# Performance work log

Measured on AMD Instinct MI355X. Metric: run time of the kernel, lower is better.

## Reference

```python
import jax, jax.numpy as jnp
import numpy as np

L, D, H, HD, M = 4096, 1024, 16, 64, 4096
EPS = 1e-5


def setup_inputs() -> dict:
    key = jax.random.key(0)
    ks = jax.random.split(key, 12)
    hidden_states = jax.random.normal(ks[0], (L, D), dtype=jnp.float32)
    cu_seqlens = jnp.arange(5, dtype=jnp.int32) * (L // 4)  # [0,1024,2048,3072,4096]
    # rope freqs as cos/sin of random angles: (L, HD//2, 2)
    angles = jax.random.uniform(ks[1], (L, HD // 2), dtype=jnp.float32) * (2.0 * np.pi)
    rope_freqs = jnp.stack([jnp.cos(angles), jnp.sin(angles)], axis=-1)
    s = 0.02
    params = {
        "ln0_g": jnp.ones((D,), jnp.float32), "ln0_b": jnp.zeros((D,), jnp.float32),
        "ln1_g": jnp.ones((D,), jnp.float32), "ln1_b": jnp.zeros((D,), jnp.float32),
        "w_qkv": jax.random.normal(ks[2], (D, 3 * D), jnp.float32) * s,
        "w_o":   jax.random.normal(ks[3], (D, D), jnp.float32) * s,
        "w_fc0": jax.random.normal(ks[4], (D, M), jnp.float32) * s,
        "b_fc0": jnp.zeros((M,), jnp.float32),
        "w_fc1": jax.random.normal(ks[5], (M, D), jnp.float32) * s,
        "b_fc1": jnp.zeros((D,), jnp.float32),
    }
    return {"hidden_states": hidden_states, "cu_seqlens": cu_seqlens, "rope_freqs": rope_freqs, **params}


def _layernorm(x, g, b):
    mu = jnp.mean(x, axis=-1, keepdims=True)
    var = jnp.var(x, axis=-1, keepdims=True)
    return (x - mu) * jax.lax.rsqrt(var + EPS) * g + b


def _apply_rope(x, fc):
    # x: (L, H, HD); fc: (L, HD//2, 2) -> broadcast over heads
    xr = x.reshape(L, H, HD // 2, 2)
    a, b = xr[..., 0], xr[..., 1]
    c, s = fc[:, None, :, 0], fc[:, None, :, 1]
    out = jnp.stack([a * c - b * s, a * s + b * c], axis=-1)
    return out.reshape(L, H, HD)


def reference(hidden_states, cu_seqlens, rope_freqs, ln0_g, ln0_b, ln1_g, ln1_b,
              w_qkv, w_o, w_fc0, b_fc0, w_fc1, b_fc1):
    residual = hidden_states
    x = _layernorm(hidden_states, ln0_g, ln0_b)
    qkv = (x @ w_qkv).reshape(L, 3, H, HD)
    q, k, v = qkv[:, 0], qkv[:, 1], qkv[:, 2]
    q = _apply_rope(q, rope_freqs)
    k = _apply_rope(k, rope_freqs)
    # block-diagonal mask from cu_seqlens
    seg = jnp.searchsorted(cu_seqlens[1:], jnp.arange(L, dtype=cu_seqlens.dtype), side="right")
    mask = seg[:, None] == seg[None, :]  # (L, L)
    scale = 1.0 / np.sqrt(HD)
    scores = jnp.einsum("lhd,mhd->hlm", q, k) * scale
    scores = jnp.where(mask[None], scores, jnp.float32(-1e30))
    probs = jax.nn.softmax(scores, axis=-1)
    attn = jnp.einsum("hlm,mhd->lhd", probs, v).reshape(L, D)
    attn = attn @ w_o
    h = residual + attn
    y = _layernorm(h, ln1_g, ln1_b)
    y = jax.nn.gelu(y @ w_fc0 + b_fc0, approximate=False) @ w_fc1 + b_fc1
    return h + y
```

## Files before the change

kernel.cpp:

```cpp
#include <hip/hip_runtime.h>
#include <cstdint>
#include <cmath>

#define L_ 4096
#define D_ 1024
#define H_ 16
#define HD_ 64
#define M_ 4096

typedef __bf16 bf16_t;
typedef __attribute__((ext_vector_type(8))) __bf16 bf16x8;
typedef __attribute__((ext_vector_type(4))) __bf16 bf16x4;
typedef __attribute__((ext_vector_type(4))) float f32x4;

__device__ __forceinline__ f32x4 mfma16(bf16x8 a, bf16x8 b, f32x4 c) {
    return __builtin_amdgcn_mfma_f32_16x16x32_bf16(a, b, c, 0, 0, 0);
}

__device__ __forceinline__ void gload_lds16(const bf16_t* g, bf16_t* l) {
    __builtin_amdgcn_global_load_lds(
        (const __attribute__((address_space(1))) unsigned int*)(g),
        (__attribute__((address_space(3))) unsigned int*)(l), 16, 0, 0);
}

__device__ __forceinline__ float fast_exp2(float x) {
    float r;
    asm volatile("v_exp_f32 %0, %1" : "=v"(r) : "v"(x));
    return r;
}
__device__ __forceinline__ float fast_rcp(float x) {
    float r;
    asm volatile("v_rcp_f32 %0, %1" : "=v"(r) : "v"(x));
    return r;
}
__device__ __forceinline__ float gelu_f(float v) {
    float t = v * (0.7978845608f + 0.0356774081f * v * v);
    return v * fast_rcp(1.f + fast_exp2(-2.885390082f * t));
}

__global__ __launch_bounds__(256) void ln_kernel(const float* __restrict__ x,
                                                 const float* __restrict__ g,
                                                 const float* __restrict__ b,
                                                 bf16_t* __restrict__ out) {
    int row = blockIdx.x, tid = threadIdx.x;
    int wave = tid >> 6, lane = tid & 63;
    const f32x4* xr = (const f32x4*)(x + (long)row * D_);
    f32x4 v = xr[tid];
    float s = v.x + v.y + v.z + v.w;
    __shared__ float red[8];
#pragma unroll
    for (int off = 32; off > 0; off >>= 1) s += __shfl_down(s, off, 64);
    if (lane == 0) red[wave] = s;
    __syncthreads();
    float mean = (red[0] + red[1] + red[2] + red[3]) * (1.f / 1024.f);
    float s2 = 0.f;
#pragma unroll
    for (int i = 0; i < 4; i++) { float d = v[i] - mean; s2 += d * d; }
#pragma unroll
    for (int off = 32; off > 0; off >>= 1) s2 += __shfl_down(s2, off, 64);
    __syncthreads();
    if (lane == 0) red[wave] = s2;
    __syncthreads();
    float var = (red[0] + red[1] + red[2] + red[3]) * (1.f / 1024.f);
    float rstd = rsqrtf(var + 1e-5f);
    f32x4 g4 = ((const f32x4*)g)[tid];
    f32x4 b4 = ((const f32x4*)b)[tid];
    bf16x4 o;
#pragma unroll
    for (int i = 0; i < 4; i++) o[i] = (bf16_t)((v[i] - mean) * rstd * g4[i] + b4[i]);
    *(bf16x4*)(out + (long)row * D_ + tid * 4) = o;
}

__global__ __launch_bounds__(256) void transpose_all(
    const float* __restrict__ w_qkv, const float* __restrict__ w_o,
    const float* __restrict__ w_fc0, const float* __restrict__ w_fc1,
    bf16_t* __restrict__ t_qkv, bf16_t* __restrict__ t_o,
    bf16_t* __restrict__ t_fc0, bf16_t* __restrict__ t_fc1) {
    __shared__ float t[32][33];
    int bidx = blockIdx.x;
    const float* W;
    bf16_t* Wt;
    int K, N, tile;
    if (bidx < 3072) { W = w_qkv; Wt = t_qkv; K = 1024; N = 3072; tile = bidx; }
    else if (bidx < 4096) { W = w_o; Wt = t_o; K = 1024; N = 1024; tile = bidx - 3072; }
    else if (bidx < 8192) { W = w_fc0; Wt = t_fc0; K = 1024; N = 4096; tile = bidx - 4096; }
    else { W = w_fc1; Wt = t_fc1; K = 4096; N = 1024; tile = bidx - 8192; }
    int nt = N >> 5;
    int n0 = (tile % nt) * 32, k0 = (tile / nt) * 32;
    int tx = threadIdx.x & 31, ty = threadIdx.x >> 5;
#pragma unroll
    for (int r = 0; r < 32; r += 8)
        t[ty + r][tx] = W[(long)(k0 + ty + r) * N + n0 + tx];
    __syncthreads();
#pragma unroll
    for (int r = 0; r < 32; r += 8)
        Wt[(long)(n0 + ty + r) * K + k0 + tx] = (bf16_t)t[tx][ty + r];
}

__global__ __launch_bounds__(256) void vt_kernel(const bf16_t* __restrict__ qkv,
                                                 bf16_t* __restrict__ Vt) {
    __shared__ bf16_t t[32][33];
    int l0 = blockIdx.x * 32, c0 = blockIdx.y * 32;
    int tx = threadIdx.x & 31, ty = threadIdx.x >> 5;
#pragma unroll
    for (int r = 0; r < 32; r += 8)
        t[ty + r][tx] = qkv[(long)(l0 + ty + r) * 3072 + 2048 + c0 + tx];
    __syncthreads();
#pragma unroll
    for (int r = 0; r < 32; r += 8)
        Vt[(long)(c0 + ty + r) * 4096 + l0 + tx] = t[tx][ty + r];
}

__global__ __launch_bounds__(256) void rope_kernel(bf16_t* __restrict__ qkv,
                                                   const float* __restrict__ freqs) {
    const float k1 = 0.125f * 1.44269504089f;
    int idx = blockIdx.x * 256 + threadIdx.x;
    int g = idx & 7;
    int h = (idx >> 3) & 15;
    int l = idx >> 7;
    const float* f = freqs + (long)l * 64 + g * 8;
    f32x4 f0 = ((const f32x4*)f)[0];
    f32x4 f1 = ((const f32x4*)f)[1];
    float c[4] = {f0.x, f0.z, f1.x, f1.z};
    float s[4] = {f0.y, f0.w, f1.y, f1.w};
    bf16_t* qp = qkv + (long)l * 3072 + h * 64 + g * 8;
    bf16x8 q = *(bf16x8*)qp;
    bf16x8 k = *(bf16x8*)(qp + 1024);
    bf16x8 qo, ko;
#pragma unroll
    for (int e = 0; e < 4; e++) {
        float a = (float)q[2 * e], b = (float)q[2 * e + 1];
        qo[2 * e] = (bf16_t)((a * c[e] - b * s[e]) * k1);
        qo[2 * e + 1] = (bf16_t)((a * s[e] + b * c[e]) * k1);
        a = (float)k[2 * e]; b = (float)k[2 * e + 1];
        ko[2 * e] = (bf16_t)(a * c[e] - b * s[e]);
        ko[2 * e + 1] = (bf16_t)(a * s[e] + b * c[e]);
    }
    *(bf16x8*)qp = qo;
    *(bf16x8*)(qp + 1024) = ko;
}

template <int EPI, int GN, int SWBN, int SWBM>
__global__ __launch_bounds__(256) void gemm_bt(const bf16_t* __restrict__ A,
                                               const bf16_t* __restrict__ Bt,
                                               int M, int N, int K,
                                               bf16_t* __restrict__ outB,
                                               const float* __restrict__ bias) {
    __shared__ __align__(16) bf16_t As[128 * 64];
    __shared__ __align__(16) bf16_t Bs[128 * 64];
    int tid = threadIdx.x;
    int wave = tid >> 6, lane = tid & 63;
    int quad = lane >> 4, l16 = lane & 15;
    int wr = wave >> 1, wc = wave & 1;

    int g = blockIdx.x & 7, w = blockIdx.x >> 3;
    int gn_idx = g % GN, gm_idx = g / GN;
    int bn_i = gn_idx * SWBN + (w % SWBN);
    int bm_i = gm_idx * SWBM + (w / SWBN);
    long bm = (long)bm_i * 128, bn = (long)bn_i * 128;

    f32x4 acc[4][4];
#pragma unroll
    for (int i = 0; i < 4; i++)
#pragma unroll
        for (int j = 0; j < 4; j++) acc[i][j] = (f32x4){0.f, 0.f, 0.f, 0.f};

    int lr = lane >> 3;
    int sc = (lane & 7) ^ (lr & 7);
    const bf16_t* a_base = A + (bm + wave * 32 + lr) * (long)K + sc * 8;
    const bf16_t* b_base = Bt + (bn + wave * 32 + lr) * (long)K + sc * 8;

    for (int k0 = 0; k0 < K; k0 += 64) {
        __syncthreads();
#pragma unroll
        for (int i = 0; i < 4; i++) {
            gload_lds16(a_base + k0 + (long)(8 * i) * K, &As[(wave * 32 + 8 * i) * 64]);
            gload_lds16(b_base + k0 + (long)(8 * i) * K, &Bs[(wave * 32 + 8 * i) * 64]);
        }
        __builtin_amdgcn_s_waitcnt(0);
        __syncthreads();

#pragma unroll
        for (int h = 0; h < 2; h++) {
            int sl = (h * 4 + quad) ^ (l16 & 7);
            bf16x8 af[4], bfr[4];
#pragma unroll
            for (int i = 0; i < 4; i++) {
                af[i] = *(const bf16x8*)&As[(wr * 64 + i * 16 + l16) * 64 + sl * 8];
                bfr[i] = *(const bf16x8*)&Bs[(wc * 64 + i * 16 + l16) * 64 + sl * 8];
            }
#pragma unroll
            for (int i = 0; i < 4; i++)
#pragma unroll
                for (int j = 0; j < 4; j++)
                    acc[i][j] = mfma16(af[i], bfr[j], acc[i][j]);
        }
    }

    long base_row = bm + wr * 64;
    long base_col = bn + wc * 64;
#pragma unroll
    for (int i = 0; i < 4; i++)
#pragma unroll
        for (int j = 0; j < 4; j++)
#pragma unroll
            for (int r = 0; r < 4; r++) {
                long row = base_row + i * 16 + quad * 4 + r;
                long col = base_col + j * 16 + l16;
                long idx = row * (long)N + col;
                float v = acc[i][j][r];
                if (EPI == 0) {
                    outB[idx] = (bf16_t)v;
                } else {
                    v += bias[col];
                    outB[idx] = (bf16_t)gelu_f(v);
                }
            }
}

__global__ __launch_bounds__(256) void gemm_splitk_store(const bf16_t* __restrict__ A,
                                                         const bf16_t* __restrict__ Bt,
                                                         int M, int N, int K, int Kc,
                                                         bf16_t* __restrict__ P) {
    __shared__ __align__(16) bf16_t As[128 * 64];
    __shared__ __align__(16) bf16_t Bs[128 * 64];
    int tid = threadIdx.x;
    int wave = tid >> 6, lane = tid & 63;
    int quad = lane >> 4, l16 = lane & 15;
    int wr = wave >> 1, wc = wave & 1;

    int g = blockIdx.x & 7, w = blockIdx.x >> 3;
    int z = g & 3, bm_hi = g >> 2;
    int bn_i = w & 7, bm_i = bm_hi * 16 + (w >> 3);
    long bm = (long)bm_i * 128, bn = (long)bn_i * 128;
    int kbeg = z * Kc, kend = kbeg + Kc;
    bf16_t* myP = P + (long)z * M * N;

    f32x4 acc[4][4];
#pragma unroll
    for (int i = 0; i < 4; i++)
#pragma unroll
        for (int j = 0; j < 4; j++) acc[i][j] = (f32x4){0.f, 0.f, 0.f, 0.f};

    int lr = lane >> 3;
    int sc = (lane & 7) ^ (lr & 7);
    const bf16_t* a_base = A + (bm + wave * 32 + lr) * (long)K + sc * 8;
    const bf16_t* b_base = Bt + (bn + wave * 32 + lr) * (long)K + sc * 8;

    for (int k0 = kbeg; k0 < kend; k0 += 64) {
        __syncthreads();
#pragma unroll
        for (int i = 0; i < 4; i++) {
            gload_lds16(a_base + k0 + (long)(8 * i) * K, &As[(wave * 32 + 8 * i) * 64]);
            gload_lds16(b_base + k0 + (long)(8 * i) * K, &Bs[(wave * 32 + 8 * i) * 64]);
        }
        __builtin_amdgcn_s_waitcnt(0);
        __syncthreads();

#pragma unroll
        for (int h = 0; h < 2; h++) {
            int sl = (h * 4 + quad) ^ (l16 & 7);
            bf16x8 af[4], bfr[4];
#pragma unroll
            for (int i = 0; i < 4; i++) {
                af[i] = *(const bf16x8*)&As[(wr * 64 + i * 16 + l16) * 64 + sl * 8];
                bfr[i] = *(const bf16x8*)&Bs[(wc * 64 + i * 16 + l16) * 64 + sl * 8];
            }
#pragma unroll
            for (int i = 0; i < 4; i++)
#pragma unroll
                for (int j = 0; j < 4; j++)
                    acc[i][j] = mfma16(af[i], bfr[j], acc[i][j]);
        }
    }

    long base_row = bm + wr * 64;
    long base_col = bn + wc * 64;
#pragma unroll
    for (int i = 0; i < 4; i++)
#pragma unroll
        for (int j = 0; j < 4; j++)
#pragma unroll
            for (int r = 0; r < 4; r++) {
                long row = base_row + i * 16 + quad * 4 + r;
                long col = base_col + j * 16 + l16;
                myP[row * (long)N + col] = (bf16_t)acc[i][j][r];
            }
}

__global__ __launch_bounds__(256) void reduce_fc1(const bf16_t* __restrict__ P,
                                                  const float* __restrict__ bias,
                                                  float* __restrict__ out) {
    long i = (long)blockIdx.x * 256 + threadIdx.x;
    f32x4 b = ((const f32x4*)bias)[i & 255];
    f32x4 v = ((f32x4*)out)[i];
#pragma unroll
    for (int z = 0; z < 4; z++) {
        bf16x4 p = ((const bf16x4*)(P + (long)z * L_ * D_))[i];
#pragma unroll
        for (int e = 0; e < 4; e++) v[e] += (float)p[e];
    }
    v.x += b.x; v.y += b.y; v.z += b.z; v.w += b.w;
    ((f32x4*)out)[i] = v;
}

__global__ __launch_bounds__(256) void gemm_bt64_res(const bf16_t* __restrict__ A,
                                                     const bf16_t* __restrict__ Bt,
                                                     int M, int N, int K,
                                                     float* __restrict__ outF,
                                                     const float* __restrict__ res) {
    __shared__ __align__(16) bf16_t As[128 * 64];
    __shared__ __align__(16) bf16_t Bs[64 * 64];
    int tid = threadIdx.x;
    int wave = tid >> 6, lane = tid & 63;
    int quad = lane >> 4, l16 = lane & 15;

    int g = blockIdx.x & 7, w = blockIdx.x >> 3;
    int bn_i = w & 15, bm_i = g * 4 + (w >> 4);
    long bm = (long)bm_i * 128, bn = (long)bn_i * 64;

    f32x4 acc[2][4];
#pragma unroll
    for (int i = 0; i < 2; i++)
#pragma unroll
        for (int j = 0; j < 4; j++) acc[i][j] = (f32x4){0.f, 0.f, 0.f, 0.f};

    int lr = lane >> 3;
    int sc = (lane & 7) ^ (lr & 7);
    const bf16_t* a_base = A + (bm + wave * 32 + lr) * (long)K + sc * 8;
    const bf16_t* b_base = Bt + (bn + wave * 16 + lr) * (long)K + sc * 8;

    for (int k0 = 0; k0 < K; k0 += 64) {
        __syncthreads();
#pragma unroll
        for (int i = 0; i < 4; i++)
            gload_lds16(a_base + k0 + (long)(8 * i) * K, &As[(wave * 32 + 8 * i) * 64]);
#pragma unroll
        for (int i = 0; i < 2; i++)
            gload_lds16(b_base + k0 + (long)(8 * i) * K, &Bs[(wave * 16 + 8 * i) * 64]);
        __builtin_amdgcn_s_waitcnt(0);
        __syncthreads();

#pragma unroll
        for (int h = 0; h < 2; h++) {
            int sl = (h * 4 + quad) ^ (l16 & 7);
            bf16x8 af[2], bfr[4];
#pragma unroll
            for (int i = 0; i < 2; i++)
                af[i] = *(const bf16x8*)&As[(wave * 32 + i * 16 + l16) * 64 + sl * 8];
#pragma unroll
            for (int j = 0; j < 4; j++)
                bfr[j] = *(const bf16x8*)&Bs[(j * 16 + l16) * 64 + sl * 8];
#pragma unroll
            for (int i = 0; i < 2; i++)
#pragma unroll
                for (int j = 0; j < 4; j++)
                    acc[i][j] = mfma16(af[i], bfr[j], acc[i][j]);
        }
    }

#pragma unroll
    for (int i = 0; i < 2; i++)
#pragma unroll
        for (int j = 0; j < 4; j++)
#pragma unroll
            for (int r = 0; r < 4; r++) {
                long row = bm + wave * 32 + i * 16 + quad * 4 + r;
                long col = bn + j * 16 + l16;
                long idx = row * (long)N + col;
                outF[idx] = acc[i][j][r] + res[idx];
            }
}

__global__ __launch_bounds__(256) void attn_kernel(const bf16_t* __restrict__ qkv,
                                                   const bf16_t* __restrict__ Vt,
                                                   const int* __restrict__ cu,
                                                   bf16_t* __restrict__ out) {
    __shared__ __align__(16) bf16_t QPs[4 * 16 * 72];
    __shared__ __align__(16) bf16_t Ks[64 * 64];
    __shared__ __align__(16) bf16_t Vs[64 * 64];

    int tid = threadIdx.x, wave = tid >> 6, lane = tid & 63;
    int quad = lane >> 4, l16 = lane & 15;
    int qt = blockIdx.x, head = blockIdx.y, seg = blockIdx.z;
    int s0 = cu[seg], s1 = cu[seg + 1];
    int r0 = s0 + qt * 64;
    const long hoff = (long)head * 64;

    bf16_t* Qs = QPs;
    bf16_t* Psw = &QPs[wave * 16 * 72];

    int lr = lane >> 3;
    int sc = (lane & 7) ^ (lr & 7);
    int sl0 = (0 * 4 + quad) ^ (l16 & 7);
    int sl1 = (1 * 4 + quad) ^ (l16 & 7);

#pragma unroll
    for (int i = 0; i < 2; i++) {
        int row = wave * 16 + i * 8 + lr;
        gload_lds16(qkv + (long)(r0 + row) * 3072 + hoff + sc * 8,
                    &Qs[(wave * 16 + i * 8) * 64]);
    }
    __builtin_amdgcn_s_waitcnt(0);
    __syncthreads();
    bf16x8 aq0 = *(const bf16x8*)&Qs[(wave * 16 + l16) * 64 + sl0 * 8];
    bf16x8 aq1 = *(const bf16x8*)&Qs[(wave * 16 + l16) * 64 + sl1 * 8];

    bf16x8 ones;
#pragma unroll
    for (int e = 0; e < 8; e++) ones[e] = (bf16_t)1.0f;

    f32x4 o[4];
#pragma unroll
    for (int j = 0; j < 4; j++) o[j] = (f32x4){0.f, 0.f, 0.f, 0.f};
    f32x4 lacc = (f32x4){0.f, 0.f, 0.f, 0.f};

    for (int kt = s0; kt < s1; kt += 64) {
        __syncthreads();
#pragma unroll
        for (int i = 0; i < 2; i++) {
            int row = wave * 16 + i * 8 + lr;
            gload_lds16(qkv + (long)(kt + row) * 3072 + 1024 + hoff + sc * 8,
                        &Ks[(wave * 16 + i * 8) * 64]);
            gload_lds16(Vt + (hoff + row) * (long)4096 + kt + sc * 8,
                        &Vs[(wave * 16 + i * 8) * 64]);
        }
        __builtin_amdgcn_s_waitcnt(0);
        __syncthreads();

        f32x4 sacc[4];
#pragma unroll
        for (int j = 0; j < 4; j++) sacc[j] = (f32x4){0.f, 0.f, 0.f, 0.f};
#pragma unroll
        for (int j = 0; j < 4; j++) {
            bf16x8 b0 = *(const bf16x8*)&Ks[(j * 16 + l16) * 64 + sl0 * 8];
            bf16x8 b1 = *(const bf16x8*)&Ks[(j * 16 + l16) * 64 + sl1 * 8];
            sacc[j] = mfma16(aq0, b0, sacc[j]);
            sacc[j] = mfma16(aq1, b1, sacc[j]);
        }

#pragma unroll
        for (int j = 0; j < 4; j++)
#pragma unroll
            for (int r = 0; r < 4; r++)
                Psw[(quad * 4 + r) * 72 + j * 16 + l16] = (bf16_t)fast_exp2(sacc[j][r]);

        __builtin_amdgcn_s_waitcnt(0);

        bf16x8 ap0 = *(const bf16x8*)&Psw[l16 * 72 + 0 * 32 + quad * 8];
        bf16x8 ap1 = *(const bf16x8*)&Psw[l16 * 72 + 1 * 32 + quad * 8];
#pragma unroll
        for (int j2 = 0; j2 < 4; j2++) {
            bf16x8 b0 = *(const bf16x8*)&Vs[(j2 * 16 + l16) * 64 + sl0 * 8];
            bf16x8 b1 = *(const bf16x8*)&Vs[(j2 * 16 + l16) * 64 + sl1 * 8];
            o[j2] = mfma16(ap0, b0, o[j2]);
            o[j2] = mfma16(ap1, b1, o[j2]);
        }
        lacc = mfma16(ap0, ones, lacc);
        lacc = mfma16(ap1, ones, lacc);
    }

#pragma unroll
    for (int r = 0; r < 4; r++) {
        float inv = fast_rcp(lacc[r]);
        int row = r0 + wave * 16 + quad * 4 + r;
#pragma unroll
        for (int j2 = 0; j2 < 4; j2++)
            out[(long)row * 1024 + head * 64 + j2 * 16 + l16] = (bf16_t)(o[j2][r] * inv);
    }
}

extern "C" void kernel_launch(void* const* d_in, const int* in_sizes, int n_in,
                              void* d_out, int out_size, void* d_ws, size_t ws_size,
                              hipStream_t stream) {
    const float* hidden = (const float*)d_in[0];
    const int* cu = (const int*)d_in[1];
    const float* freqs = (const float*)d_in[2];
    const float* ln0_g = (const float*)d_in[3];
    const float* ln0_b = (const float*)d_in[4];
    const float* ln1_g = (const float*)d_in[5];
    const float* ln1_b = (const float*)d_in[6];
    const float* w_qkv = (const float*)d_in[7];
    const float* w_o = (const float*)d_in[8];
    const float* w_fc0 = (const float*)d_in[9];
    const float* b_fc0 = (const float*)d_in[10];
    const float* w_fc1 = (const float*)d_in[11];
    const float* b_fc1 = (const float*)d_in[12];
    float* out = (float*)d_out;

    char* ws = (char*)d_ws;
    bf16_t* qkv = (bf16_t*)(ws);
    bf16_t* attn = (bf16_t*)(ws + ((size_t)24 << 20));
    bf16_t* act = (bf16_t*)(ws);
    bf16_t* x_bf = (bf16_t*)(ws + ((size_t)32 << 20));
    bf16_t* Vt = x_bf;
    bf16_t* y_bf = x_bf;
    bf16_t* fc1p = (bf16_t*)(ws + ((size_t)40 << 20));
    bf16_t* wqkvT = (bf16_t*)(ws + ((size_t)72 << 20));
    bf16_t* woT = (bf16_t*)(ws + ((size_t)78 << 20));
    bf16_t* wfc0T = (bf16_t*)(ws + ((size_t)80 << 20));
    bf16_t* wfc1T = (bf16_t*)(ws + ((size_t)88 << 20));
    float* h = out;

    transpose_all<<<12288, 256, 0, stream>>>(w_qkv, w_o, w_fc0, w_fc1,
                                             wqkvT, woT, wfc0T, wfc1T);

    ln_kernel<<<L_, 256, 0, stream>>>(hidden, ln0_g, ln0_b, x_bf);

    gemm_bt<0, 2, 12, 8><<<768, 256, 0, stream>>>(
        x_bf, wqkvT, L_, 3072, 1024, qkv, nullptr);

    rope_kernel<<<(L_ * H_ * 8) / 256, 256, 0, stream>>>(qkv, freqs);
    vt_kernel<<<dim3(4096 / 32, 1024 / 32), 256, 0, stream>>>(qkv, Vt);

    attn_kernel<<<dim3(16, 16, 4), 256, 0, stream>>>(qkv, Vt, cu, attn);

    gemm_bt64_res<<<512, 256, 0, stream>>>(
        attn, woT, L_, 1024, 1024, h, hidden);

    ln_kernel<<<L_, 256, 0, stream>>>(h, ln1_g, ln1_b, y_bf);

    gemm_bt<2, 4, 8, 16><<<1024, 256, 0, stream>>>(
        y_bf, wfc0T, L_, 4096, 1024, act, b_fc0);

    gemm_splitk_store<<<1024, 256, 0, stream>>>(
        act, wfc1T, L_, 1024, 4096, 1024, fc1p);
    reduce_fc1<<<(L_ * D_ / 4) / 256, 256, 0, stream>>>(fc1p, b_fc1, out);
}
```

Before: 342.2 us.

## Process 128-key tiles in attention, remap block indices, narrow waitcnt masks

The attention kernel now loads two 64-key K/V tiles per iteration into doubled LDS buffers, which halves the number of barrier/load rounds per key sequence. The 3D grid is flattened into a 1D grid whose index mapping groups 8 consecutive blocks per head set, presumably to improve cache locality or XCD distribution. All s_waitcnt(0) calls are replaced with masks that wait only on vector-memory or only on LDS counters, so the waits no longer also drain unrelated counters. In exchange the kernel uses more LDS and handles fewer blocks per iteration, which could reduce occupancy.

```diff
diff --git a/kernel.cpp b/kernel.cpp
--- a/kernel.cpp
+++ b/kernel.cpp
@@ -12,6 +12,9 @@
 typedef __attribute__((ext_vector_type(8))) __bf16 bf16x8;
 typedef __attribute__((ext_vector_type(4))) __bf16 bf16x4;
 typedef __attribute__((ext_vector_type(4))) float f32x4;
+
+#define WAIT_VM0 0x0f70
+#define WAIT_LGKM0 0xc07f
 
 __device__ __forceinline__ f32x4 mfma16(bf16x8 a, bf16x8 b, f32x4 c) {
     return __builtin_amdgcn_mfma_f32_16x16x32_bf16(a, b, c, 0, 0, 0);
@@ -177,7 +180,7 @@
             gload_lds16(a_base + k0 + (long)(8 * i) * K, &As[(wave * 32 + 8 * i) * 64]);
             gload_lds16(b_base + k0 + (long)(8 * i) * K, &Bs[(wave * 32 + 8 * i) * 64]);
         }
-        __builtin_amdgcn_s_waitcnt(0);
+        __builtin_amdgcn_s_waitcnt(WAIT_VM0);
         __syncthreads();
 
 #pragma unroll
@@ -254,7 +257,7 @@
             gload_lds16(a_base + k0 + (long)(8 * i) * K, &As[(wave * 32 + 8 * i) * 64]);
             gload_lds16(b_base + k0 + (long)(8 * i) * K, &Bs[(wave * 32 + 8 * i) * 64]);
         }
-        __builtin_amdgcn_s_waitcnt(0);
+        __builtin_amdgcn_s_waitcnt(WAIT_VM0);
         __syncthreads();
 
 #pragma unroll
@@ -338,7 +341,7 @@
 #pragma unroll
         for (int i = 0; i < 2; i++)
             gload_lds16(b_base + k0 + (long)(8 * i) * K, &Bs[(wave * 16 + 8 * i) * 64]);
-        __builtin_amdgcn_s_waitcnt(0);
+        __builtin_amdgcn_s_waitcnt(WAIT_VM0);
         __syncthreads();
 
 #pragma unroll
@@ -377,12 +380,16 @@
                                                    const int* __restrict__ cu,
                                                    bf16_t* __restrict__ out) {
     __shared__ __align__(16) bf16_t QPs[4 * 16 * 72];
-    __shared__ __align__(16) bf16_t Ks[64 * 64];
-    __shared__ __align__(16) bf16_t Vs[64 * 64];
+    __shared__ __align__(16) bf16_t Ks[2][64 * 64];
+    __shared__ __align__(16) bf16_t Vs[2][64 * 64];
 
     int tid = threadIdx.x, wave = tid >> 6, lane = tid & 63;
     int quad = lane >> 4, l16 = lane & 15;
-    int qt = blockIdx.x, head = blockIdx.y, seg = blockIdx.z;
+
+    int g = blockIdx.x & 7, w = blockIdx.x >> 3;
+    int head = (w & 1) * 8 + g;
+    int qt = (w >> 1) & 15;
+    int seg = w >> 5;
     int s0 = cu[seg], s1 = cu[seg + 1];
     int r0 = s0 + qt * 64;
     const long hoff = (long)head * 64;
@@ -401,7 +408,7 @@
         gload_lds16(qkv + (long)(r0 + row) * 3072 + hoff + sc * 8,
                     &Qs[(wave * 16 + i * 8) * 64]);
     }
-    __builtin_amdgcn_s_waitcnt(0);
+    __builtin_amdgcn_s_waitcnt(WAIT_VM0);
     __syncthreads();
     bf16x8 aq0 = *(const bf16x8*)&Qs[(wave * 16 + l16) * 64 + sl0 * 8];
     bf16x8 aq1 = *(const bf16x8*)&Qs[(wave * 16 + l16) * 64 + sl1 * 8];
@@ -415,49 +422,54 @@
     for (int j = 0; j < 4; j++) o[j] = (f32x4){0.f, 0.f, 0.f, 0.f};
     f32x4 lacc = (f32x4){0.f, 0.f, 0.f, 0.f};
 
-    for (int kt = s0; kt < s1; kt += 64) {
+    for (int kt = s0; kt < s1; kt += 128) {
         __syncthreads();
 #pragma unroll
         for (int i = 0; i < 2; i++) {
             int row = wave * 16 + i * 8 + lr;
-            gload_lds16(qkv + (long)(kt + row) * 3072 + 1024 + hoff + sc * 8,
-                        &Ks[(wave * 16 + i * 8) * 64]);
-            gload_lds16(Vt + (hoff + row) * (long)4096 + kt + sc * 8,
-                        &Vs[(wave * 16 + i * 8) * 64]);
-        }
-        __builtin_amdgcn_s_waitcnt(0);
-        __syncthreads();
-
-        f32x4 sacc[4];
-#pragma unroll
-        for (int j = 0; j < 4; j++) sacc[j] = (f32x4){0.f, 0.f, 0.f, 0.f};
-#pragma unroll
-        for (int j = 0; j < 4; j++) {
-            bf16x8 b0 = *(const bf16x8*)&Ks[(j * 16 + l16) * 64 + sl0 * 8];
-            bf16x8 b1 = *(const bf16x8*)&Ks[(j * 16 + l16) * 64 + sl1 * 8];
-            sacc[j] = mfma16(aq0, b0, sacc[j]);
-            sacc[j] = mfma16(aq1, b1, sacc[j]);
-        }
-
-#pragma unroll
-        for (int j = 0; j < 4; j++)
-#pragma unroll
-            for (int r = 0; r < 4; r++)
-                Psw[(quad * 4 + r) * 72 + j * 16 + l16] = (bf16_t)fast_exp2(sacc[j][r]);
-
-        __builtin_amdgcn_s_waitcnt(0);
-
-        bf16x8 ap0 = *(const bf16x8*)&Psw[l16 * 72 + 0 * 32 + quad * 8];
-        bf16x8 ap1 = *(const bf16x8*)&Psw[l16 * 72 + 1 * 32 + quad * 8];
-#pragma unroll
-        for (int j2 = 0; j2 < 4; j2++) {
-            bf16x8 b0 = *(const bf16x8*)&Vs[(j2 * 16 + l16) * 64 + sl0 * 8];
-            bf16x8 b1 = *(const bf16x8*)&Vs[(j2 * 16 + l16) * 64 + sl1 * 8];
-            o[j2] = mfma16(ap0, b0, o[j2]);
-            o[j2] = mfma16(ap1, b1, o[j2]);
-        }
-        lacc = mfma16(ap0, ones, lacc);
-        lacc = mfma16(ap1, ones, lacc);
+            long kr0 = (long)(kt + row) * 3072 + 1024 + hoff + sc * 8;
+            gload_lds16(qkv + kr0, &Ks[0][(wave * 16 + i * 8) * 64]);
+            gload_lds16(qkv + kr0 + (long)64 * 3072, &Ks[1][(wave * 16 + i * 8) * 64]);
+            long vr0 = (hoff + row) * (long)4096 + kt + sc * 8;
+            gload_lds16(Vt + vr0, &Vs[0][(wave * 16 + i * 8) * 64]);
+            gload_lds16(Vt + vr0 + 64, &Vs[1][(wave * 16 + i * 8) * 64]);
+        }
+        __builtin_amdgcn_s_waitcnt(WAIT_VM0);
+        __syncthreads();
+
+#pragma unroll
+        for (int half = 0; half < 2; half++) {
+            f32x4 sacc[4];
+#pragma unroll
+            for (int j = 0; j < 4; j++) sacc[j] = (f32x4){0.f, 0.f, 0.f, 0.f};
+#pragma unroll
+            for (int j = 0; j < 4; j++) {
+                bf16x8 b0 = *(const bf16x8*)&Ks[half][(j * 16 + l16) * 64 + sl0 * 8];
+                bf16x8 b1 = *(const bf16x8*)&Ks[half][(j * 16 + l16) * 64 + sl1 * 8];
+                sacc[j] = mfma16(aq0, b0, sacc[j]);
+                sacc[j] = mfma16(aq1, b1, sacc[j]);
+            }
+
+#pragma unroll
+            for (int j = 0; j < 4; j++)
+#pragma unroll
+                for (int r = 0; r < 4; r++)
+                    Psw[(quad * 4 + r) * 72 + j * 16 + l16] = (bf16_t)fast_exp2(sacc[j][r]);
+
+            __builtin_amdgcn_s_waitcnt(WAIT_LGKM0);
+
+            bf16x8 ap0 = *(const bf16x8*)&Psw[l16 * 72 + 0 * 32 + quad * 8];
+            bf16x8 ap1 = *(const bf16x8*)&Psw[l16 * 72 + 1 * 32 + quad * 8];
+#pragma unroll
+            for (int j2 = 0; j2 < 4; j2++) {
+                bf16x8 b0 = *(const bf16x8*)&Vs[half][(j2 * 16 + l16) * 64 + sl0 * 8];
+                bf16x8 b1 = *(const bf16x8*)&Vs[half][(j2 * 16 + l16) * 64 + sl1 * 8];
+                o[j2] = mfma16(ap0, b0, o[j2]);
+                o[j2] = mfma16(ap1, b1, o[j2]);
+            }
+            lacc = mfma16(ap0, ones, lacc);
+            lacc = mfma16(ap1, ones, lacc);
+        }
     }
 
 #pragma unroll
@@ -513,7 +525,7 @@
     rope_kernel<<<(L_ * H_ * 8) / 256, 256, 0, stream>>>(qkv, freqs);
     vt_kernel<<<dim3(4096 / 32, 1024 / 32), 256, 0, stream>>>(qkv, Vt);
 
-    attn_kernel<<<dim3(16, 16, 4), 256, 0, stream>>>(qkv, Vt, cu, attn);
+    attn_kernel<<<1024, 256, 0, stream>>>(qkv, Vt, cu, attn);
 
     gemm_bt64_res<<<512, 256, 0, stream>>>(
         attn, woT, L_, 1024, 1024, h, hidden);
```

Measured after the change: 341.9 us. Within noise of the previous version (-0.1%).
